# Optimization experiments

Hardware: AMD Instinct MI355X
Metric: run time of the kernel (lower is better)

## Reference

```python
import jax, jax.numpy as jnp
import numpy as np

N, T, H, D, E, P, R = 50000, 16, 512, 256, 200000, 100000, 3
LN_EPS = 1e-5
BN_EPS = 1e-5


def setup_inputs() -> dict:
    key = jax.random.key(0)
    ks = jax.random.split(key, 32)
    ri = lambda k, shape, hi: jax.random.randint(k, shape, 0, hi)
    rn = lambda k, shape, scale=0.05: (jax.random.normal(k, shape, dtype=jnp.float32) * scale)
    return {
        "node_type_ids": ri(ks[0], (N,), T),
        "src0": ri(ks[1], (E,), N), "dst0": ri(ks[2], (E,), N),
        "src1": ri(ks[3], (E,), N), "dst1": ri(ks[4], (E,), N),
        "src2": ri(ks[5], (E,), N), "dst2": ri(ks[6], (E,), N),
        "pairs": ri(ks[7], (2, P), N),
        "degrees": ri(ks[8], (N,), 100),
        "node_emb": rn(ks[9], (N, H)),
        "type_emb": rn(ks[10], (T, H)),
        "w_loop_in": rn(ks[11], (H, H)),
        "w_rel_in": rn(ks[12], (R, H, H)),
        "w_loop_res": rn(ks[13], (H, H)),
        "w_rel_res": rn(ks[14], (R, H, H)),
        "ln_g": jnp.ones((H,), jnp.float32),
        "ln_b": jnp.zeros((H,), jnp.float32),
        "w_loop_out": rn(ks[15], (H, D)),
        "w_rel_out": rn(ks[16], (R, H, D)),
        "lp_w1": rn(ks[17], (3 * D, D)),
        "lp_b1": jnp.zeros((D,), jnp.float32),
        "bn_g": jnp.ones((D,), jnp.float32),
        "bn_b": jnp.zeros((D,), jnp.float32),
        "bn_mean": jnp.zeros((D,), jnp.float32),
        "bn_var": jnp.ones((D,), jnp.float32),
        "lp_w2": rn(ks[18], (D, 1)),
        "lp_b2": jnp.zeros((1,), jnp.float32),
        "alpha": jnp.float32(0.1),
        "beta": jnp.float32(0.1),
    }


def _rgcn(x, loop_w, rel_w, srcs, dsts):
    # out = x @ W_loop + sum_r (A_r @ x) @ W_r ; A_r unweighted COO -> segment_sum
    out = x @ loop_w
    for r in range(R):
        msg = jax.ops.segment_sum(x[srcs[r]], dsts[r], num_segments=x.shape[0])
        out = out + msg @ rel_w[r]
    return out


def _layernorm(h, g, b):
    mu = h.mean(-1, keepdims=True)
    var = h.var(-1, keepdims=True)
    return (h - mu) * jax.lax.rsqrt(var + LN_EPS) * g + b


def reference(node_type_ids, src0, dst0, src1, dst1, src2, dst2, pairs, degrees,
              node_emb, type_emb, w_loop_in, w_rel_in, w_loop_res, w_rel_res,
              ln_g, ln_b, w_loop_out, w_rel_out, lp_w1, lp_b1, bn_g, bn_b,
              bn_mean, bn_var, lp_w2, lp_b2, alpha, beta):
    srcs = (src0, src1, src2)
    dsts = (dst0, dst1, dst2)
    # encode
    x = node_emb + type_emb[node_type_ids]          # [N, H]
    x = jax.nn.relu(_rgcn(x, w_loop_in, w_rel_in, srcs, dsts))
    h = _rgcn(x, w_loop_res, w_rel_res, srcs, dsts)
    h = jax.nn.relu(_layernorm(h, ln_g, ln_b))      # dropout p=0 -> identity
    x = x + h
    z = _rgcn(x, w_loop_out, w_rel_out, srcs, dsts)  # [N, D]
    # score
    src_z = z[pairs[0]]                              # [P, D]
    dst_z = z[pairs[1]]
    src_deg = jnp.clip(degrees[pairs[0]], 1).astype(jnp.float32)
    dst_deg = jnp.clip(degrees[pairs[1]], 1).astype(jnp.float32)
    feats = jnp.concatenate([src_z, dst_z, src_z * dst_z], axis=-1)  # [P, 3D]
    h1 = jax.nn.relu(feats @ lp_w1 + lp_b1)
    # BatchNorm1d in eval mode: running stats
    h1 = (h1 - bn_mean) * jax.lax.rsqrt(bn_var + BN_EPS) * bn_g + bn_b
    mlp_score = (h1 @ lp_w2 + lp_b2).squeeze(-1)     # [P]
    base = mlp_score - jax.nn.relu(alpha) * jnp.log(src_deg) - jax.nn.relu(beta) * jnp.log(dst_deg)
    return base / (jnp.sqrt(src_deg) * jnp.sqrt(dst_deg) + 1e-8)
```

## Files before the change

kernel.cpp:

```cpp
#include <hip/hip_runtime.h>

typedef __attribute__((ext_vector_type(8))) _Float16 half8;
typedef __attribute__((ext_vector_type(4))) _Float16 half4;
typedef __attribute__((ext_vector_type(4))) float f32x4;

static __device__ __forceinline__ void gload16(const void* g, void* l) {
  __builtin_amdgcn_global_load_lds((const __attribute__((address_space(1))) void*)g,
                                   (__attribute__((address_space(3))) void*)l, 16, 0, 0);
}

__global__ void k_encode(const float* __restrict__ emb, const float* __restrict__ temb,
                         const int* __restrict__ tids, _Float16* __restrict__ x, int n) {
  int i = blockIdx.x * 256 + threadIdx.x;
  if (i >= n * 64) return;
  int node = i >> 6, c = (i & 63) << 3;
  const float* e = emb + (size_t)node * 512 + c;
  const float* t = temb + (size_t)tids[node] * 512 + c;
  float4 a0 = *(const float4*)e, a1 = *(const float4*)(e + 4);
  float4 b0 = *(const float4*)t, b1 = *(const float4*)(t + 4);
  half8 o;
  o[0] = (_Float16)(a0.x + b0.x); o[1] = (_Float16)(a0.y + b0.y);
  o[2] = (_Float16)(a0.z + b0.z); o[3] = (_Float16)(a0.w + b0.w);
  o[4] = (_Float16)(a1.x + b1.x); o[5] = (_Float16)(a1.y + b1.y);
  o[6] = (_Float16)(a1.z + b1.z); o[7] = (_Float16)(a1.w + b1.w);
  *(half8*)(x + (size_t)node * 512 + c) = o;
}

__global__ void k_zero(int* __restrict__ p, int n) {
  int i = blockIdx.x * 256 + threadIdx.x;
  if (i < n) p[i] = 0;
}

__global__ void k_hist(const int* __restrict__ d0, const int* __restrict__ d1,
                       const int* __restrict__ d2, int* __restrict__ counts, int E, int Np1) {
  int e = blockIdx.x * 256 + threadIdx.x;
  if (e >= E) return;
  int r = blockIdx.y;
  const int* d = (r == 0) ? d0 : ((r == 1) ? d1 : d2);
  atomicAdd(&counts[r * Np1 + d[e] + 1], 1);
}

__global__ void k_scan(const int* __restrict__ counts, int* __restrict__ rowp, int n) {
  __shared__ int wsum[16];
  int r = blockIdx.x;
  const int* c = counts + (size_t)r * n;
  int* o = rowp + (size_t)r * n;
  int lane = threadIdx.x & 63, w = threadIdx.x >> 6;
  int off = 0;
  for (int base = 0; base < n; base += 1024) {
    int i = base + threadIdx.x;
    int v = (i < n) ? c[i] : 0;
    int sc = v;
    #pragma unroll
    for (int d = 1; d < 64; d <<= 1) {
      int t = __shfl_up(sc, (unsigned)d);
      if (lane >= d) sc += t;
    }
    if (lane == 63) wsum[w] = sc;
    __syncthreads();
    int wo = 0, tot = 0;
    #pragma unroll
    for (int ww = 0; ww < 16; ++ww) {
      int s = wsum[ww];
      if (ww < w) wo += s;
      tot += s;
    }
    if (i < n) o[i] = sc + wo + off;
    off += tot;
    __syncthreads();
  }
}

__global__ void k_copy(const int* __restrict__ a, int* __restrict__ b, int n) {
  int i = blockIdx.x * 256 + threadIdx.x;
  if (i < n) b[i] = a[i];
}

__global__ void k_fill(const int* __restrict__ s0, const int* __restrict__ s1, const int* __restrict__ s2,
                       const int* __restrict__ d0, const int* __restrict__ d1, const int* __restrict__ d2,
                       int* __restrict__ cursor, int* __restrict__ col_src, int E, int Np1) {
  int e = blockIdx.x * 256 + threadIdx.x;
  if (e >= E) return;
  int r = blockIdx.y;
  const int* dp = (r == 0) ? d0 : ((r == 1) ? d1 : d2);
  const int* sp = (r == 0) ? s0 : ((r == 1) ? s1 : s2);
  int pos = atomicAdd(&cursor[r * Np1 + dp[e]], 1);
  if (pos >= 0 && pos < E) col_src[(size_t)r * E + pos] = sp[e];
}

__global__ void k_aggregate(const _Float16* __restrict__ x, _Float16* __restrict__ agg,
                            const int* __restrict__ rowp, const int* __restrict__ col_src,
                            int N, int E) {
  int wid = (blockIdx.x * 256 + threadIdx.x) >> 6;
  int lane = threadIdx.x & 63;
  if (wid >= 3 * N) return;
  int r = wid / N;
  int n = wid - r * N;
  int beg = rowp[r * (N + 1) + n], end = rowp[r * (N + 1) + n + 1];
  const int* cs = col_src + (size_t)r * E;
  float acc[8] = {0, 0, 0, 0, 0, 0, 0, 0};
  for (int e = beg; e < end; ++e) {
    int s = cs[e];
    half8 v = *(const half8*)(x + (size_t)s * 512 + lane * 8);
    #pragma unroll
    for (int j = 0; j < 8; ++j) acc[j] += (float)v[j];
  }
  half8 o;
  #pragma unroll
  for (int j = 0; j < 8; ++j) o[j] = (_Float16)acc[j];
  *(half8*)(agg + (size_t)n * 1536 + r * 512 + lane * 8) = o;
}

__global__ void k_transpose(const float* __restrict__ Bl, const float* __restrict__ Br,
                            _Float16* __restrict__ Bt, int No, int K) {
  __shared__ float tile[64][65];
  int k0 = blockIdx.x * 64, n0 = blockIdx.y * 64;
  int nl = threadIdx.x & 63, kb = threadIdx.x >> 6;
  #pragma unroll
  for (int i = 0; i < 16; ++i) {
    int kl = kb + i * 4;
    int krow = k0 + kl;
    float v = (krow < 512) ? Bl[(size_t)krow * No + n0 + nl]
                           : Br[(size_t)(krow - 512) * No + n0 + nl];
    tile[kl][nl] = v;
  }
  __syncthreads();
  int kl = threadIdx.x & 63, nb = threadIdx.x >> 6;
  #pragma unroll
  for (int i = 0; i < 16; ++i) {
    int n2 = nb + i * 4;
    Bt[(size_t)(n0 + n2) * K + k0 + kl] = (_Float16)tile[kl][n2];
  }
}

__global__ __launch_bounds__(256) void k_gemm_rgcn(
    const _Float16* __restrict__ Ain, const _Float16* __restrict__ Aagg,
    const _Float16* __restrict__ Bt, _Float16* __restrict__ C,
    int M, int Ncols, int K, int relu, int S, int T) {
  __shared__ __align__(16) _Float16 As[128 * 64];
  __shared__ __align__(16) _Float16 Bs[128 * 64];
  int lin = blockIdx.x;
  int grp = lin / (8 * T);
  int rmd = lin - grp * 8 * T;
  int c = rmd >> 3, x = rmd & 7;
  int s = grp * 8 + x;
  if (s >= S) return;
  int bm0 = s * 128, bn0 = c * 128;

  int tid = threadIdx.x;
  int lane = tid & 63, wv = tid >> 6;
  int wm = wv & 1, wn = wv >> 1;
  int l16 = lane & 15, quad = lane >> 4;

  int rl8 = lane >> 3;
  int gs = (lane & 7) ^ rl8;
  int rA[4], rB[4];
  const _Float16* pa[4];
  const _Float16* pb[4];
  _Float16* ldA[4];
  _Float16* ldB[4];
  #pragma unroll
  for (int q = 0; q < 4; ++q) {
    int chunk = wv * 4 + q;
    int rl = chunk * 8 + rl8;
    int ra = bm0 + rl; if (ra >= M) ra = M - 1;
    rA[q] = ra;
    rB[q] = bn0 + rl;
    pa[q] = Ain + (size_t)ra * 512 + gs * 8;
    pb[q] = Bt + (size_t)rB[q] * K + gs * 8;
    ldA[q] = &As[chunk * 8 * 64];
    ldB[q] = &Bs[chunk * 8 * 64];
  }

  f32x4 acc[4][4];
  #pragma unroll
  for (int i = 0; i < 4; ++i)
    #pragma unroll
    for (int j = 0; j < 4; ++j) acc[i][j] = (f32x4){0.f, 0.f, 0.f, 0.f};

  for (int k0 = 0; k0 < K; k0 += 64) {
    if (k0 == 512) {
      #pragma unroll
      for (int q = 0; q < 4; ++q) pa[q] = Aagg + (size_t)rA[q] * 1536 + gs * 8;
    }
    __syncthreads();
    #pragma unroll
    for (int q = 0; q < 4; ++q) gload16(pa[q], ldA[q]);
    #pragma unroll
    for (int q = 0; q < 4; ++q) gload16(pb[q], ldB[q]);
    __syncthreads();
    #pragma unroll
    for (int sb = 0; sb < 2; ++sb) {
      half8 af[4], bf[4];
      int slot = ((sb * 4 + quad) ^ (l16 & 7)) * 8;
      #pragma unroll
      for (int i = 0; i < 4; ++i)
        af[i] = *(const half8*)&As[(wm * 64 + i * 16 + l16) * 64 + slot];
      #pragma unroll
      for (int j = 0; j < 4; ++j)
        bf[j] = *(const half8*)&Bs[(wn * 64 + j * 16 + l16) * 64 + slot];
      #pragma unroll
      for (int i = 0; i < 4; ++i)
        #pragma unroll
        for (int j = 0; j < 4; ++j)
          acc[i][j] = __builtin_amdgcn_mfma_f32_16x16x32_f16(af[i], bf[j], acc[i][j], 0, 0, 0);
    }
    #pragma unroll
    for (int q = 0; q < 4; ++q) { pa[q] += 64; pb[q] += 64; }
  }

  #pragma unroll
  for (int i = 0; i < 4; ++i)
    #pragma unroll
    for (int j = 0; j < 4; ++j)
      #pragma unroll
      for (int rg = 0; rg < 4; ++rg) {
        int row = bm0 + wm * 64 + i * 16 + quad * 4 + rg;
        int col = bn0 + wn * 64 + j * 16 + l16;
        if (row < M) {
          float v = acc[i][j][rg];
          if (relu) v = fmaxf(v, 0.f);
          C[(size_t)row * Ncols + col] = (_Float16)v;
        }
      }
}

#define LSTR 40

__global__ __launch_bounds__(256) void k_gemm_link(
    const _Float16* __restrict__ z, const int* __restrict__ pairs,
    const _Float16* __restrict__ Bt,
    const float* __restrict__ b1, const float* __restrict__ bng, const float* __restrict__ bnb,
    const float* __restrict__ bnm, const float* __restrict__ bnv,
    _Float16* __restrict__ h1, int P, int K) {
  __shared__ __align__(16) _Float16 As[128 * LSTR];
  __shared__ __align__(16) _Float16 Bs[128 * LSTR];
  int tid = threadIdx.x;
  int bn0 = blockIdx.x * 128, bm0 = blockIdx.y * 128;
  int lane = tid & 63, wv = tid >> 6;
  int wm = wv & 1, wn = wv >> 1;
  int l16 = lane & 15, quad = lane >> 4;
  int srow = tid >> 1, scs = (tid & 1) * 16;
  int p = bm0 + srow; if (p >= P) p = P - 1;
  int sp = pairs[p], dp = pairs[P + p];
  const _Float16* zs = z + (size_t)sp * 256;
  const _Float16* zd = z + (size_t)dp * 256;
  int bgn = bn0 + srow;

  f32x4 acc[4][4];
  #pragma unroll
  for (int i = 0; i < 4; ++i)
    #pragma unroll
    for (int j = 0; j < 4; ++j) acc[i][j] = (f32x4){0.f, 0.f, 0.f, 0.f};

  for (int k0 = 0; k0 < K; k0 += 32) {
    __syncthreads();
    int seg = k0 >> 8;
    int kk = (k0 & 255) + scs;
    __attribute__((aligned(16))) _Float16 tmp[16];
    if (seg == 0) {
      *(uint4*)tmp = *(const uint4*)(zs + kk);
      *(uint4*)(tmp + 8) = *(const uint4*)(zs + kk + 8);
    } else if (seg == 1) {
      *(uint4*)tmp = *(const uint4*)(zd + kk);
      *(uint4*)(tmp + 8) = *(const uint4*)(zd + kk + 8);
    } else {
      half8 u0 = *(const half8*)(zs + kk), u1 = *(const half8*)(zs + kk + 8);
      half8 v0 = *(const half8*)(zd + kk), v1 = *(const half8*)(zd + kk + 8);
      #pragma unroll
      for (int j = 0; j < 8; ++j) {
        tmp[j] = (_Float16)((float)u0[j] * (float)v0[j]);
        tmp[j + 8] = (_Float16)((float)u1[j] * (float)v1[j]);
      }
    }
    *(uint4*)&As[srow * LSTR + scs] = *(const uint4*)tmp;
    *(uint4*)&As[srow * LSTR + scs + 8] = *(const uint4*)(tmp + 8);
    {
      const _Float16* src = Bt + (size_t)bgn * K + k0 + scs;
      *(uint4*)&Bs[srow * LSTR + scs] = *(const uint4*)src;
      *(uint4*)&Bs[srow * LSTR + scs + 8] = *(const uint4*)(src + 8);
    }
    __syncthreads();
    half8 af[4], bf[4];
    #pragma unroll
    for (int i = 0; i < 4; ++i)
      af[i] = *(const half8*)&As[(wm * 64 + i * 16 + l16) * LSTR + quad * 8];
    #pragma unroll
    for (int j = 0; j < 4; ++j)
      bf[j] = *(const half8*)&Bs[(wn * 64 + j * 16 + l16) * LSTR + quad * 8];
    #pragma unroll
    for (int i = 0; i < 4; ++i)
      #pragma unroll
      for (int j = 0; j < 4; ++j)
        acc[i][j] = __builtin_amdgcn_mfma_f32_16x16x32_f16(af[i], bf[j], acc[i][j], 0, 0, 0);
  }

  #pragma unroll
  for (int i = 0; i < 4; ++i)
    #pragma unroll
    for (int j = 0; j < 4; ++j) {
      int col = bn0 + wn * 64 + j * 16 + l16;
      float bb1 = b1[col], m = bnm[col], rs = rsqrtf(bnv[col] + 1e-5f);
      float gg = bng[col], bb = bnb[col];
      #pragma unroll
      for (int rg = 0; rg < 4; ++rg) {
        int row = bm0 + wm * 64 + i * 16 + quad * 4 + rg;
        if (row < P) {
          float v = fmaxf(acc[i][j][rg] + bb1, 0.f);
          v = (v - m) * rs * gg + bb;
          h1[(size_t)row * 256 + col] = (_Float16)v;
        }
      }
    }
}

__global__ void k_ln_res(const _Float16* __restrict__ h, const _Float16* __restrict__ x1,
                         const float* __restrict__ g, const float* __restrict__ b,
                         _Float16* __restrict__ out, int N) {
  int wid = (blockIdx.x * 256 + threadIdx.x) >> 6;
  int lane = threadIdx.x & 63;
  if (wid >= N) return;
  int c = lane * 8;
  half8 hv = *(const half8*)(h + (size_t)wid * 512 + c);
  float hf[8];
  float s = 0.f, sq = 0.f;
  #pragma unroll
  for (int j = 0; j < 8; ++j) {
    hf[j] = (float)hv[j];
    s += hf[j];
    sq += hf[j] * hf[j];
  }
  #pragma unroll
  for (int off = 32; off; off >>= 1) {
    s += __shfl_down(s, (unsigned)off);
    sq += __shfl_down(sq, (unsigned)off);
  }
  s = __shfl(s, 0); sq = __shfl(sq, 0);
  float mu = s * (1.f / 512.f);
  float var = sq * (1.f / 512.f) - mu * mu;
  float rs = rsqrtf(var + 1e-5f);
  float4 g0 = *(const float4*)(g + c), g1 = *(const float4*)(g + c + 4);
  float4 b0 = *(const float4*)(b + c), b1 = *(const float4*)(b + c + 4);
  float gf[8] = {g0.x, g0.y, g0.z, g0.w, g1.x, g1.y, g1.z, g1.w};
  float bf[8] = {b0.x, b0.y, b0.z, b0.w, b1.x, b1.y, b1.z, b1.w};
  half8 xv = *(const half8*)(x1 + (size_t)wid * 512 + c);
  half8 o;
  #pragma unroll
  for (int j = 0; j < 8; ++j) {
    float xw = (float)xv[j];
    o[j] = (_Float16)(xw + fmaxf((hf[j] - mu) * rs * gf[j] + bf[j], 0.f));
  }
  *(half8*)(out + (size_t)wid * 512 + c) = o;
}

__global__ void k_score(const _Float16* __restrict__ h1, const float* __restrict__ w2,
                        const float* __restrict__ b2, const int* __restrict__ pairs,
                        const int* __restrict__ degrees, const float* __restrict__ alpha,
                        const float* __restrict__ beta, float* __restrict__ out, int P) {
  int wid = (blockIdx.x * 256 + threadIdx.x) >> 6;
  int lane = threadIdx.x & 63;
  if (wid >= P) return;
  int c = lane * 4;
  half4 hv = *(const half4*)(h1 + (size_t)wid * 256 + c);
  float4 wv = *(const float4*)(w2 + c);
  float s = (float)hv[0] * wv.x + (float)hv[1] * wv.y + (float)hv[2] * wv.z + (float)hv[3] * wv.w;
  #pragma unroll
  for (int off = 32; off; off >>= 1) s += __shfl_down(s, (unsigned)off);
  if (lane == 0) {
    int sp = pairs[wid], dp = pairs[P + wid];
    float sd = (float)max(degrees[sp], 1);
    float dd = (float)max(degrees[dp], 1);
    float base = s + b2[0] - fmaxf(alpha[0], 0.f) * logf(sd) - fmaxf(beta[0], 0.f) * logf(dd);
    out[wid] = base / (sqrtf(sd) * sqrtf(dd) + 1e-8f);
  }
}

extern "C" void kernel_launch(void* const* d_in, const int* in_sizes, int n_in,
                              void* d_out, int out_size, void* d_ws, size_t ws_size,
                              hipStream_t stream) {
  const int N = 50000, E = 200000, P = 100000;
  const int Np1 = N + 1;
  const int* node_type = (const int*)d_in[0];
  const int* src0 = (const int*)d_in[1]; const int* dst0 = (const int*)d_in[2];
  const int* src1 = (const int*)d_in[3]; const int* dst1 = (const int*)d_in[4];
  const int* src2 = (const int*)d_in[5]; const int* dst2 = (const int*)d_in[6];
  const int* pairs = (const int*)d_in[7];
  const int* degrees = (const int*)d_in[8];
  const float* node_emb = (const float*)d_in[9];
  const float* type_emb = (const float*)d_in[10];
  const float* w_loop_in = (const float*)d_in[11];
  const float* w_rel_in = (const float*)d_in[12];
  const float* w_loop_res = (const float*)d_in[13];
  const float* w_rel_res = (const float*)d_in[14];
  const float* ln_g = (const float*)d_in[15];
  const float* ln_b = (const float*)d_in[16];
  const float* w_loop_out = (const float*)d_in[17];
  const float* w_rel_out = (const float*)d_in[18];
  const float* lp_w1 = (const float*)d_in[19];
  const float* lp_b1 = (const float*)d_in[20];
  const float* bn_g = (const float*)d_in[21];
  const float* bn_b = (const float*)d_in[22];
  const float* bn_mean = (const float*)d_in[23];
  const float* bn_var = (const float*)d_in[24];
  const float* lp_w2 = (const float*)d_in[25];
  const float* lp_b2 = (const float*)d_in[26];
  const float* alpha = (const float*)d_in[27];
  const float* beta = (const float*)d_in[28];
  float* out = (float*)d_out;

  char* ws = (char*)d_ws;
  size_t off = 0;
  auto alloc = [&](size_t bytes) {
    void* p = ws + off;
    off = (off + bytes + 255) & ~(size_t)255;
    return p;
  };
  _Float16* xb0 = (_Float16*)alloc((size_t)N * 512 * 2);
  _Float16* xb1 = (_Float16*)alloc((size_t)N * 512 * 2);
  _Float16* agg = (_Float16*)alloc((size_t)N * 1536 * 2);
  _Float16* Bt = (_Float16*)alloc((size_t)512 * 2048 * 2);
  int* counts = (int*)alloc((size_t)3 * Np1 * 4);
  int* rowp = (int*)alloc((size_t)3 * Np1 * 4);
  int* cursor = (int*)alloc((size_t)3 * Np1 * 4);
  int* col_src = (int*)alloc((size_t)3 * E * 4);
  if (off > ws_size) return;

  _Float16* z = xb1;
  _Float16* h1 = agg;

  k_zero<<<(3 * Np1 + 255) / 256, 256, 0, stream>>>(counts, 3 * Np1);
  dim3 gE((E + 255) / 256, 3);
  k_hist<<<gE, 256, 0, stream>>>(dst0, dst1, dst2, counts, E, Np1);
  k_scan<<<3, 1024, 0, stream>>>(counts, rowp, Np1);
  k_copy<<<(3 * Np1 + 255) / 256, 256, 0, stream>>>(rowp, cursor, 3 * Np1);
  k_fill<<<gE, 256, 0, stream>>>(src0, src1, src2, dst0, dst1, dst2, cursor, col_src, E, Np1);

  k_encode<<<(N * 64 + 255) / 256, 256, 0, stream>>>(node_emb, type_emb, node_type, xb0, N);

  int aggBlocks = (3 * N + 3) / 4;
  const int S = (N + 127) / 128;
  int blocks4 = ((S + 7) / 8) * 8 * 4;
  int blocks2 = ((S + 7) / 8) * 8 * 2;

  k_aggregate<<<aggBlocks, 256, 0, stream>>>(xb0, agg, rowp, col_src, N, E);
  k_transpose<<<dim3(32, 8), 256, 0, stream>>>(w_loop_in, w_rel_in, Bt, 512, 2048);
  k_gemm_rgcn<<<blocks4, 256, 0, stream>>>(xb0, agg, Bt, xb1, N, 512, 2048, 1, S, 4);

  k_aggregate<<<aggBlocks, 256, 0, stream>>>(xb1, agg, rowp, col_src, N, E);
  k_transpose<<<dim3(32, 8), 256, 0, stream>>>(w_loop_res, w_rel_res, Bt, 512, 2048);
  k_gemm_rgcn<<<blocks4, 256, 0, stream>>>(xb1, agg, Bt, xb0, N, 512, 2048, 0, S, 4);

  k_ln_res<<<(N + 3) / 4, 256, 0, stream>>>(xb0, xb1, ln_g, ln_b, xb0, N);

  k_aggregate<<<aggBlocks, 256, 0, stream>>>(xb0, agg, rowp, col_src, N, E);
  k_transpose<<<dim3(32, 4), 256, 0, stream>>>(w_loop_out, w_rel_out, Bt, 256, 2048);
  k_gemm_rgcn<<<blocks2, 256, 0, stream>>>(xb0, agg, Bt, z, N, 256, 2048, 0, S, 2);

  k_transpose<<<dim3(12, 4), 256, 0, stream>>>(lp_w1, lp_w1 + 512 * 256, Bt, 256, 768);
  dim3 gl(2, (P + 127) / 128);
  k_gemm_link<<<gl, 256, 0, stream>>>(z, pairs, Bt, lp_b1, bn_g, bn_b, bn_mean, bn_var, h1, P, 768);

  k_score<<<(P + 3) / 4, 256, 0, stream>>>(h1, lp_w2, lp_b2, pairs, degrees, alpha, beta, out, P);
}
```

Before: 1.134 ms.

## Enlarge RGCN GEMM tile to 256 rows, merge transposes, fuse relation aggregation

The RGCN GEMM now uses 512-thread blocks covering 256 output rows by 128 columns, so each B tile loaded into shared memory is reused across twice as many rows. The four separate weight transposes become one launch writing into four dedicated buffers. The aggregation kernel now has one wavefront per node loop over all three relations, with a one-ahead prefetch of the next source index. The larger GEMM tile raises shared memory per block and halves the number of blocks, which may lower occupancy or leave the grid less balanced across CUs.

```diff
diff --git a/kernel.cpp b/kernel.cpp
--- a/kernel.cpp
+++ b/kernel.cpp
@@ -93,28 +93,43 @@
                             int N, int E) {
   int wid = (blockIdx.x * 256 + threadIdx.x) >> 6;
   int lane = threadIdx.x & 63;
-  if (wid >= 3 * N) return;
-  int r = wid / N;
-  int n = wid - r * N;
-  int beg = rowp[r * (N + 1) + n], end = rowp[r * (N + 1) + n + 1];
-  const int* cs = col_src + (size_t)r * E;
-  float acc[8] = {0, 0, 0, 0, 0, 0, 0, 0};
-  for (int e = beg; e < end; ++e) {
-    int s = cs[e];
-    half8 v = *(const half8*)(x + (size_t)s * 512 + lane * 8);
-    #pragma unroll
-    for (int j = 0; j < 8; ++j) acc[j] += (float)v[j];
-  }
-  half8 o;
-  #pragma unroll
-  for (int j = 0; j < 8; ++j) o[j] = (_Float16)acc[j];
-  *(half8*)(agg + (size_t)n * 1536 + r * 512 + lane * 8) = o;
-}
-
-__global__ void k_transpose(const float* __restrict__ Bl, const float* __restrict__ Br,
-                            _Float16* __restrict__ Bt, int No, int K) {
+  if (wid >= N) return;
+  int Np1 = N + 1;
+  #pragma unroll
+  for (int r = 0; r < 3; ++r) {
+    int beg = rowp[r * Np1 + wid], end = rowp[r * Np1 + wid + 1];
+    const int* cs = col_src + (size_t)r * E;
+    float acc[8] = {0, 0, 0, 0, 0, 0, 0, 0};
+    int sn = (beg < end) ? cs[beg] : 0;
+    for (int e = beg; e < end; ++e) {
+      int sc = sn;
+      if (e + 1 < end) sn = cs[e + 1];
+      half8 v = *(const half8*)(x + (size_t)sc * 512 + lane * 8);
+      #pragma unroll
+      for (int j = 0; j < 8; ++j) acc[j] += (float)v[j];
+    }
+    half8 o;
+    #pragma unroll
+    for (int j = 0; j < 8; ++j) o[j] = (_Float16)acc[j];
+    *(half8*)(agg + (size_t)wid * 1536 + r * 512 + lane * 8) = o;
+  }
+}
+
+__global__ void k_transpose_all(const float* __restrict__ wli, const float* __restrict__ wri,
+                                const float* __restrict__ wlr, const float* __restrict__ wrr,
+                                const float* __restrict__ wlo, const float* __restrict__ wro,
+                                const float* __restrict__ lpw1,
+                                _Float16* __restrict__ Bti, _Float16* __restrict__ Btr,
+                                _Float16* __restrict__ Bto, _Float16* __restrict__ Btl) {
   __shared__ float tile[64][65];
+  int zi = blockIdx.z;
+  const float* Bl; const float* Br; _Float16* Bt; int No, K;
+  if (zi == 0)      { Bl = wli;  Br = wri;            Bt = Bti; No = 512; K = 2048; }
+  else if (zi == 1) { Bl = wlr;  Br = wrr;            Bt = Btr; No = 512; K = 2048; }
+  else if (zi == 2) { Bl = wlo;  Br = wro;            Bt = Bto; No = 256; K = 2048; }
+  else              { Bl = lpw1; Br = lpw1 + 512*256; Bt = Btl; No = 256; K = 768;  }
   int k0 = blockIdx.x * 64, n0 = blockIdx.y * 64;
+  if (k0 >= K || n0 >= No) return;
   int nl = threadIdx.x & 63, kb = threadIdx.x >> 6;
   #pragma unroll
   for (int i = 0; i < 16; ++i) {
@@ -133,11 +148,11 @@
   }
 }
 
-__global__ __launch_bounds__(256) void k_gemm_rgcn(
+__global__ __launch_bounds__(512) void k_gemm_rgcn(
     const _Float16* __restrict__ Ain, const _Float16* __restrict__ Aagg,
     const _Float16* __restrict__ Bt, _Float16* __restrict__ C,
     int M, int Ncols, int K, int relu, int S, int T) {
-  __shared__ __align__(16) _Float16 As[128 * 64];
+  __shared__ __align__(16) _Float16 As[256 * 64];
   __shared__ __align__(16) _Float16 Bs[128 * 64];
   int lin = blockIdx.x;
   int grp = lin / (8 * T);
@@ -145,30 +160,35 @@
   int c = rmd >> 3, x = rmd & 7;
   int s = grp * 8 + x;
   if (s >= S) return;
-  int bm0 = s * 128, bn0 = c * 128;
+  int bm0 = s * 256, bn0 = c * 128;
 
   int tid = threadIdx.x;
   int lane = tid & 63, wv = tid >> 6;
-  int wm = wv & 1, wn = wv >> 1;
+  int wm = wv & 3, wn = wv >> 2;
   int l16 = lane & 15, quad = lane >> 4;
 
   int rl8 = lane >> 3;
   int gs = (lane & 7) ^ rl8;
-  int rA[4], rB[4];
+
+  int rA[4];
   const _Float16* pa[4];
-  const _Float16* pb[4];
+  const _Float16* pb[2];
   _Float16* ldA[4];
-  _Float16* ldB[4];
+  _Float16* ldB[2];
   #pragma unroll
   for (int q = 0; q < 4; ++q) {
     int chunk = wv * 4 + q;
     int rl = chunk * 8 + rl8;
     int ra = bm0 + rl; if (ra >= M) ra = M - 1;
     rA[q] = ra;
-    rB[q] = bn0 + rl;
     pa[q] = Ain + (size_t)ra * 512 + gs * 8;
-    pb[q] = Bt + (size_t)rB[q] * K + gs * 8;
     ldA[q] = &As[chunk * 8 * 64];
+  }
+  #pragma unroll
+  for (int q = 0; q < 2; ++q) {
+    int chunk = wv * 2 + q;
+    int rl = chunk * 8 + rl8;
+    pb[q] = Bt + (size_t)(bn0 + rl) * K + gs * 8;
     ldB[q] = &Bs[chunk * 8 * 64];
   }
 
@@ -187,7 +207,7 @@
     #pragma unroll
     for (int q = 0; q < 4; ++q) gload16(pa[q], ldA[q]);
     #pragma unroll
-    for (int q = 0; q < 4; ++q) gload16(pb[q], ldB[q]);
+    for (int q = 0; q < 2; ++q) gload16(pb[q], ldB[q]);
     __syncthreads();
     #pragma unroll
     for (int sb = 0; sb < 2; ++sb) {
@@ -206,7 +226,9 @@
           acc[i][j] = __builtin_amdgcn_mfma_f32_16x16x32_f16(af[i], bf[j], acc[i][j], 0, 0, 0);
     }
     #pragma unroll
-    for (int q = 0; q < 4; ++q) { pa[q] += 64; pb[q] += 64; }
+    for (int q = 0; q < 4; ++q) pa[q] += 64;
+    #pragma unroll
+    for (int q = 0; q < 2; ++q) pb[q] += 64;
   }
 
   #pragma unroll
@@ -418,7 +440,10 @@
   _Float16* xb0 = (_Float16*)alloc((size_t)N * 512 * 2);
   _Float16* xb1 = (_Float16*)alloc((size_t)N * 512 * 2);
   _Float16* agg = (_Float16*)alloc((size_t)N * 1536 * 2);
-  _Float16* Bt = (_Float16*)alloc((size_t)512 * 2048 * 2);
+  _Float16* Bti = (_Float16*)alloc((size_t)512 * 2048 * 2);
+  _Float16* Btr = (_Float16*)alloc((size_t)512 * 2048 * 2);
+  _Float16* Bto = (_Float16*)alloc((size_t)256 * 2048 * 2);
+  _Float16* Btl = (_Float16*)alloc((size_t)256 * 768 * 2);
   int* counts = (int*)alloc((size_t)3 * Np1 * 4);
   int* rowp = (int*)alloc((size_t)3 * Np1 * 4);
   int* cursor = (int*)alloc((size_t)3 * Np1 * 4);
@@ -427,6 +452,10 @@
 
   _Float16* z = xb1;
   _Float16* h1 = agg;
+
+  k_transpose_all<<<dim3(32, 8, 4), 256, 0, stream>>>(
+      w_loop_in, w_rel_in, w_loop_res, w_rel_res, w_loop_out, w_rel_out, lp_w1,
+      Bti, Btr, Bto, Btl);
 
   k_zero<<<(3 * Np1 + 255) / 256, 256, 0, stream>>>(counts, 3 * Np1);
   dim3 gE((E + 255) / 256, 3);
@@ -437,28 +466,24 @@
 
   k_encode<<<(N * 64 + 255) / 256, 256, 0, stream>>>(node_emb, type_emb, node_type, xb0, N);
 
-  int aggBlocks = (3 * N + 3) / 4;
-  const int S = (N + 127) / 128;
+  int aggBlocks = (N + 3) / 4;
+  const int S = (N + 255) / 256;
   int blocks4 = ((S + 7) / 8) * 8 * 4;
   int blocks2 = ((S + 7) / 8) * 8 * 2;
 
   k_aggregate<<<aggBlocks, 256, 0, stream>>>(xb0, agg, rowp, col_src, N, E);
-  k_transpose<<<dim3(32, 8), 256, 0, stream>>>(w_loop_in, w_rel_in, Bt, 512, 2048);
-  k_gemm_rgcn<<<blocks4, 256, 0, stream>>>(xb0, agg, Bt, xb1, N, 512, 2048, 1, S, 4);
+  k_gemm_rgcn<<<blocks4, 512, 0, stream>>>(xb0, agg, Bti, xb1, N, 512, 2048, 1, S, 4);
 
   k_aggregate<<<aggBlocks, 256, 0, stream>>>(xb1, agg, rowp, col_src, N, E);
-  k_transpose<<<dim3(32, 8), 256, 0, stream>>>(w_loop_res, w_rel_res, Bt, 512, 2048);
-  k_gemm_rgcn<<<blocks4, 256, 0, stream>>>(xb1, agg, Bt, xb0, N, 512, 2048, 0, S, 4);
+  k_gemm_rgcn<<<blocks4, 512, 0, stream>>>(xb1, agg, Btr, xb0, N, 512, 2048, 0, S, 4);
 
   k_ln_res<<<(N + 3) / 4, 256, 0, stream>>>(xb0, xb1, ln_g, ln_b, xb0, N);
 
   k_aggregate<<<aggBlocks, 256, 0, stream>>>(xb0, agg, rowp, col_src, N, E);
-  k_transpose<<<dim3(32, 4), 256, 0, stream>>>(w_loop_out, w_rel_out, Bt, 256, 2048);
-  k_gemm_rgcn<<<blocks2, 256, 0, stream>>>(xb0, agg, Bt, z, N, 256, 2048, 0, S, 2);
-
-  k_transpose<<<dim3(12, 4), 256, 0, stream>>>(lp_w1, lp_w1 + 512 * 256, Bt, 256, 768);
+  k_gemm_rgcn<<<blocks2, 512, 0, stream>>>(xb0, agg, Bto, z, N, 256, 2048, 0, S, 2);
+
   dim3 gl(2, (P + 127) / 128);
-  k_gemm_link<<<gl, 256, 0, stream>>>(z, pairs, Bt, lp_b1, bn_g, bn_b, bn_mean, bn_var, h1, P, 768);
+  k_gemm_link<<<gl, 256, 0, stream>>>(z, pairs, Btl, lp_b1, bn_g, bn_b, bn_mean, bn_var, h1, P, 768);
 
   k_score<<<(P + 3) / 4, 256, 0, stream>>>(h1, lp_w2, lp_b2, pairs, degrees, alpha, beta, out, P);
 }
```

After: 1.058 ms. 6.7% less time.
